# Optimization experiments

Hardware: AMD Instinct MI355X
Metric: run time of the kernel (lower is better)

Reference implementation:

```python
import jax, jax.numpy as jnp
import numpy as np

C_IN = 256


def setup_inputs() -> dict:
    key = jax.random.key(0)
    ks = jax.random.split(key, 10)
    B, C, H, W = 1, C_IN, 96, 96
    Cq = C // 8
    s = 0.05
    return {
        "x": jax.random.normal(ks[0], (B, C, H, W), dtype=jnp.float32),
        "Wq": jax.random.normal(ks[1], (Cq, C), dtype=jnp.float32) * s,
        "bq": jax.random.normal(ks[2], (Cq,), dtype=jnp.float32) * s,
        "Wk": jax.random.normal(ks[3], (Cq, C), dtype=jnp.float32) * s,
        "bk": jax.random.normal(ks[4], (Cq,), dtype=jnp.float32) * s,
        "Wv": jax.random.normal(ks[5], (C, C), dtype=jnp.float32) * s,
        "bv": jax.random.normal(ks[6], (C,), dtype=jnp.float32) * s,
        "W6": jax.random.normal(ks[7], (C, C), dtype=jnp.float32) * s,
        "b6": jax.random.normal(ks[8], (C,), dtype=jnp.float32) * s,
        "gamma": jnp.ones((1,), dtype=jnp.float32),
    }


def reference(x, Wq, bq, Wk, bk, Wv, bv, W6, b6, gamma):
    # TRM forward (OFS just wraps it). 1x1 convs expressed as einsums.
    B, C, H, W = x.shape
    N = H * W
    scale = C ** -0.5  # 1 / sqrt(in_dim)
    xf = x.reshape(B, C, N)
    q = jnp.einsum('oc,bcn->bon', Wq, xf) + bq[None, :, None]   # (B, C/8, N)
    k = jnp.einsum('oc,bcn->bon', Wk, xf) + bk[None, :, None]   # (B, C/8, N)
    v = jnp.einsum('oc,bcn->bon', Wv, xf) + bv[None, :, None]   # (B, C,   N)
    # energy[b,n,m] = sum_c q[b,c,n] * k[b,c,m]  -> full spatial attention (B,N,N)
    energy = jnp.einsum('bcn,bcm->bnm', q, k)
    att = jax.nn.softmax(energy, axis=-1)
    # out[b,c,n] = sum_m v[b,c,m] * att[b,n,m]
    out = jnp.einsum('bcm,bnm->bcn', v, att)                    # (B, C, N)
    # torch: out.permute(2,0,1) -> (N,B,C); max/mean over C; sum; mean over B
    out_co = out.max(axis=1) + out.mean(axis=1)                 # (B, N)
    x_co = out_co.mean(axis=0).reshape(B, -1) * scale           # valid because B == 1
    x_co = jax.nn.softmax(x_co, axis=-1).reshape(B, 1, H, W)    # spatial gate
    gated = x * x_co
    y = jnp.einsum('oc,bchw->bohw', W6, gated) + b6[None, :, None, None]
    return gamma * y + x + y
```

## Files before the change

kernel.cpp:

```cpp
#include <hip/hip_runtime.h>

#define N 9216
#define CIN 256
#define DQ 32
#define NT 144
#define LOG2E 1.44269504088896340736f

typedef short short8 __attribute__((ext_vector_type(8)));
typedef float floatx4 __attribute__((ext_vector_type(4)));
typedef unsigned short ushort_t;

__device__ __forceinline__ ushort_t f2bf(float f) {
  union { float f; unsigned u; } a; a.f = f;
  unsigned u = a.u;
  u += 0x7fffu + ((u >> 16) & 1u);
  return (ushort_t)(u >> 16);
}
__device__ __forceinline__ ushort_t f2bf_fast(float f) {
  union { float f; unsigned u; } a; a.f = f;
  return (ushort_t)((a.u + 0x8000u) >> 16);
}
__device__ __forceinline__ float bf2f(ushort_t h) {
  union { unsigned u; float f; } a; a.u = ((unsigned)h) << 16;
  return a.f;
}

#define ACC4(R, W, XV)                                                   \
  acc[R][0] += (W) * (XV).x;  acc[R][1] += (W) * (XV).y;                 \
  acc[R][2] += (W) * (XV).z;  acc[R][3] += (W) * (XV).w;

__global__ __launch_bounds__(256) void qkv_kernel(
    const float* __restrict__ x,
    const float* __restrict__ Wq, const float* __restrict__ bq,
    const float* __restrict__ Wk, const float* __restrict__ bk,
    const float* __restrict__ Wv, const float* __restrict__ bv,
    ushort_t* __restrict__ qT, ushort_t* __restrict__ kT,
    ushort_t* __restrict__ vG, float* __restrict__ sumExp)
{
  if (blockIdx.x == 0 && blockIdx.y == 0 && threadIdx.x == 0) *sumExp = 0.f;

  __shared__ float xs[64][68];
  const int t = threadIdx.x;
  const int n0 = blockIdx.x * 64;
  const int oc = blockIdx.y;
  const int i = t >> 4, j = t & 15;
  const int o0 = oc * 64 + i * 4;

  const float *W0, *W1, *W2, *W3;
  float b0, b1, b2, b3;
  {
    const int o = o0;
    if (oc == 0) {
      if (o < 32) { W0 = Wq + o*CIN; W1 = Wq + (o+1)*CIN; W2 = Wq + (o+2)*CIN; W3 = Wq + (o+3)*CIN;
                    b0 = bq[o]; b1 = bq[o+1]; b2 = bq[o+2]; b3 = bq[o+3]; }
      else        { W0 = Wk + (o-32)*CIN; W1 = Wk + (o-31)*CIN; W2 = Wk + (o-30)*CIN; W3 = Wk + (o-29)*CIN;
                    b0 = bk[o-32]; b1 = bk[o-31]; b2 = bk[o-30]; b3 = bk[o-29]; }
    } else        { W0 = Wv + (o-64)*CIN; W1 = Wv + (o-63)*CIN; W2 = Wv + (o-62)*CIN; W3 = Wv + (o-61)*CIN;
                    b0 = bv[o-64]; b1 = bv[o-63]; b2 = bv[o-62]; b3 = bv[o-61]; }
  }

  float acc[4][4] = {};
  for (int cc = 0; cc < 4; ++cc) {
    {
      const int row = t >> 2, cq = t & 3;
      const float* src = x + (size_t)(cc * 64 + row) * N + n0 + cq * 16;
      float4 a0 = *(const float4*)(src + 0);
      float4 a1 = *(const float4*)(src + 4);
      float4 a2 = *(const float4*)(src + 8);
      float4 a3 = *(const float4*)(src + 12);
      float* dst = &xs[row][cq * 16];
      *(float4*)(dst + 0) = a0; *(float4*)(dst + 4)  = a1;
      *(float4*)(dst + 8) = a2; *(float4*)(dst + 12) = a3;
    }
    __syncthreads();
#pragma unroll 4
    for (int k4 = 0; k4 < 16; ++k4) {
      const float4 w0 = *(const float4*)(W0 + cc * 64 + k4 * 4);
      const float4 w1 = *(const float4*)(W1 + cc * 64 + k4 * 4);
      const float4 w2 = *(const float4*)(W2 + cc * 64 + k4 * 4);
      const float4 w3 = *(const float4*)(W3 + cc * 64 + k4 * 4);
      const float4 x0 = *(const float4*)&xs[k4 * 4 + 0][j * 4];
      const float4 x1 = *(const float4*)&xs[k4 * 4 + 1][j * 4];
      const float4 x2 = *(const float4*)&xs[k4 * 4 + 2][j * 4];
      const float4 x3 = *(const float4*)&xs[k4 * 4 + 3][j * 4];
      ACC4(0, w0.x, x0) ACC4(0, w0.y, x1) ACC4(0, w0.z, x2) ACC4(0, w0.w, x3)
      ACC4(1, w1.x, x0) ACC4(1, w1.y, x1) ACC4(1, w1.z, x2) ACC4(1, w1.w, x3)
      ACC4(2, w2.x, x0) ACC4(2, w2.y, x1) ACC4(2, w2.z, x2) ACC4(2, w2.w, x3)
      ACC4(3, w3.x, x0) ACC4(3, w3.y, x1) ACC4(3, w3.z, x2) ACC4(3, w3.w, x3)
    }
    __syncthreads();
  }

  const float bias[4] = {b0, b1, b2, b3};
#pragma unroll
  for (int r = 0; r < 4; ++r) {
    const int o = o0 + r;
#pragma unroll
    for (int c = 0; c < 4; ++c) {
      const int n = n0 + j * 4 + c;
      const float val = acc[r][c] + bias[r];
      if (oc == 0) {
        if (o < 32) qT[(size_t)n * DQ + o]        = f2bf(val * LOG2E);
        else        kT[(size_t)n * DQ + (o - 32)] = f2bf(val);
      } else        vG[(size_t)(o - 64) * N + n]  = f2bf(val);
    }
  }
}

__global__ __launch_bounds__(256, 4) void attn_kernel(
    const ushort_t* __restrict__ qT, const ushort_t* __restrict__ kT,
    const ushort_t* __restrict__ vG,
    ushort_t* __restrict__ Opart, float* __restrict__ lpart,
    int base, int rem)
{
  __shared__ ushort_t Pb[2][64][36];

  const int t = threadIdx.x;
  const int w = t >> 6;
  const int lane = t & 63;
  const int quad = lane >> 4;
  const int l15 = lane & 15;
  const int nt = blockIdx.x;
  const int s  = blockIdx.y;
  const int n0 = nt * 64;
  const int sliceIters = base + (s < rem ? 1 : 0);
  const int it0 = s * base + (s < rem ? s : rem);
  const int mbase = it0 * 32;
  const int cw = w * 64;

  short8 aq = *(const short8*)(qT + (size_t)(n0 + 16 * w + l15) * DQ + 8 * quad);

  floatx4 acc[4][4];
#pragma unroll
  for (int a2 = 0; a2 < 4; ++a2)
#pragma unroll
    for (int b2 = 0; b2 < 4; ++b2)
      acc[a2][b2] = (floatx4){0.f, 0.f, 0.f, 0.f};
  float lsum[4] = {0.f, 0.f, 0.f, 0.f};
  const floatx4 z4 = {0.f, 0.f, 0.f, 0.f};

  for (int it = 0; it < sliceIters; ++it) {
    const int m0 = mbase + it * 32;

    short8 kb0 = *(const short8*)(kT + (size_t)(m0 + l15) * DQ + 8 * quad);
    short8 kb1 = *(const short8*)(kT + (size_t)(m0 + 16 + l15) * DQ + 8 * quad);
    floatx4 s0 = __builtin_amdgcn_mfma_f32_16x16x32_bf16(aq, kb0, z4, 0, 0, 0);
    floatx4 s1 = __builtin_amdgcn_mfma_f32_16x16x32_bf16(aq, kb1, z4, 0, 0, 0);

    const ushort_t* vb = vG + (size_t)m0 + 8 * quad;
    short8 av0 = *(const short8*)(vb + (size_t)(cw +  0 + l15) * N);
    short8 av1 = *(const short8*)(vb + (size_t)(cw + 16 + l15) * N);
    short8 av2 = *(const short8*)(vb + (size_t)(cw + 32 + l15) * N);
    short8 av3 = *(const short8*)(vb + (size_t)(cw + 48 + l15) * N);

    ushort_t* pb = &Pb[it & 1][0][0];
#pragma unroll
    for (int r = 0; r < 4; ++r) {
      float p0 = exp2f(s0[r]);
      float p1 = exp2f(s1[r]);
      lsum[r] += p0 + p1;
      const int row = 16 * w + 4 * quad + r;
      pb[row * 36 + l15]      = f2bf_fast(p0);
      pb[row * 36 + 16 + l15] = f2bf_fast(p1);
    }
    __syncthreads();

#pragma unroll
    for (int b2 = 0; b2 < 4; ++b2) {
      const ushort_t* pr = pb + (b2 * 16 + l15) * 36 + 8 * quad;
      union { uint2 u2[2]; short8 v; } u;
      u.u2[0] = *(const uint2*)(pr);
      u.u2[1] = *(const uint2*)(pr + 4);
      const short8 pf = u.v;
      acc[0][b2] = __builtin_amdgcn_mfma_f32_16x16x32_bf16(av0, pf, acc[0][b2], 0, 0, 0);
      acc[1][b2] = __builtin_amdgcn_mfma_f32_16x16x32_bf16(av1, pf, acc[1][b2], 0, 0, 0);
      acc[2][b2] = __builtin_amdgcn_mfma_f32_16x16x32_bf16(av2, pf, acc[2][b2], 0, 0, 0);
      acc[3][b2] = __builtin_amdgcn_mfma_f32_16x16x32_bf16(av3, pf, acc[3][b2], 0, 0, 0);
    }
  }

#pragma unroll
  for (int r = 0; r < 4; ++r) {
    float v = lsum[r];
    v += __shfl_xor(v, 1);
    v += __shfl_xor(v, 2);
    v += __shfl_xor(v, 4);
    v += __shfl_xor(v, 8);
    lsum[r] = v;
  }
  if (l15 == 0) {
#pragma unroll
    for (int r = 0; r < 4; ++r)
      lpart[(size_t)s * N + n0 + 16 * w + 4 * quad + r] = lsum[r];
  }

  const size_t basep = ((size_t)s * NT + nt) * 256;
#pragma unroll
  for (int a2 = 0; a2 < 4; ++a2)
#pragma unroll
    for (int b2 = 0; b2 < 4; ++b2)
#pragma unroll
      for (int r = 0; r < 4; ++r) {
        const int c  = cw + a2 * 16 + 4 * quad + r;
        const int nl = b2 * 16 + l15;
        Opart[(basep + c) * 64 + nl] = f2bf(acc[a2][b2][r]);
      }
}

template<int NSL>
__global__ __launch_bounds__(1024) void cco_kernel(
    const ushort_t* __restrict__ Opart, const float* __restrict__ lpart,
    float* __restrict__ e_buf, float* __restrict__ sumExp)
{
  const int nt = blockIdx.x;
  const int t = threadIdx.x;
  const int n = t & 63, ci = t >> 6;
  float mx = -3.4e38f, sm = 0.f;
#pragma unroll
  for (int k = 0; k < 16; ++k) {
    const int c = ci * 16 + k;
    float val = 0.f;
#pragma unroll
    for (int s2 = 0; s2 < NSL; ++s2)
      val += bf2f(Opart[(((size_t)s2 * NT + nt) * 256 + c) * 64 + n]);
    mx = fmaxf(mx, val);
    sm += val;
  }
  __shared__ float rmx[16][64], rsm[16][64];
  rmx[ci][n] = mx; rsm[ci][n] = sm;
  __syncthreads();
  if (t < 64) {
    float m = rmx[0][t], s = rsm[0][t];
#pragma unroll
    for (int g = 1; g < 16; ++g) { m = fmaxf(m, rmx[g][t]); s += rsm[g][t]; }
    float l = 0.f;
#pragma unroll
    for (int s3 = 0; s3 < NSL; ++s3) l += lpart[(size_t)s3 * N + nt * 64 + t];
    const float oc = (m + s * (1.0f / 256.0f)) / l;
    const float ev = exp2f(oc * (0.0625f * LOG2E));
    e_buf[nt * 64 + t] = ev;
    float vs = ev;
    vs += __shfl_xor(vs, 1);  vs += __shfl_xor(vs, 2);
    vs += __shfl_xor(vs, 4);  vs += __shfl_xor(vs, 8);
    vs += __shfl_xor(vs, 16); vs += __shfl_xor(vs, 32);
    if (t == 0) atomicAdd(sumExp, vs);
  }
}

__global__ __launch_bounds__(256) void final_kernel(
    const float* __restrict__ x, const float* __restrict__ W6,
    const float* __restrict__ b6, const float* __restrict__ gamma,
    const float* __restrict__ e_buf, const float* __restrict__ sumExp,
    float* __restrict__ out)
{
  __shared__ float xs[64][68];
  const int t = threadIdx.x;
  const int n0 = blockIdx.x * 64;
  const int i = t >> 4, j = t & 15;
  const int o0 = blockIdx.y * 64 + i * 4;

  const float* W0 = W6 + (size_t)(o0 + 0) * CIN;
  const float* W1 = W6 + (size_t)(o0 + 1) * CIN;
  const float* W2 = W6 + (size_t)(o0 + 2) * CIN;
  const float* W3 = W6 + (size_t)(o0 + 3) * CIN;

  float acc[4][4] = {};
  for (int cc = 0; cc < 4; ++cc) {
    {
      const int row = t >> 2, cq = t & 3;
      const float* src = x + (size_t)(cc * 64 + row) * N + n0 + cq * 16;
      float4 a0 = *(const float4*)(src + 0);
      float4 a1 = *(const float4*)(src + 4);
      float4 a2 = *(const float4*)(src + 8);
      float4 a3 = *(const float4*)(src + 12);
      float* dst = &xs[row][cq * 16];
      *(float4*)(dst + 0) = a0; *(float4*)(dst + 4)  = a1;
      *(float4*)(dst + 8) = a2; *(float4*)(dst + 12) = a3;
    }
    __syncthreads();
#pragma unroll 4
    for (int k4 = 0; k4 < 16; ++k4) {
      const float4 w0 = *(const float4*)(W0 + cc * 64 + k4 * 4);
      const float4 w1 = *(const float4*)(W1 + cc * 64 + k4 * 4);
      const float4 w2 = *(const float4*)(W2 + cc * 64 + k4 * 4);
      const float4 w3 = *(const float4*)(W3 + cc * 64 + k4 * 4);
      const float4 x0 = *(const float4*)&xs[k4 * 4 + 0][j * 4];
      const float4 x1 = *(const float4*)&xs[k4 * 4 + 1][j * 4];
      const float4 x2 = *(const float4*)&xs[k4 * 4 + 2][j * 4];
      const float4 x3 = *(const float4*)&xs[k4 * 4 + 3][j * 4];
      ACC4(0, w0.x, x0) ACC4(0, w0.y, x1) ACC4(0, w0.z, x2) ACC4(0, w0.w, x3)
      ACC4(1, w1.x, x0) ACC4(1, w1.y, x1) ACC4(1, w1.z, x2) ACC4(1, w1.w, x3)
      ACC4(2, w2.x, x0) ACC4(2, w2.y, x1) ACC4(2, w2.z, x2) ACC4(2, w2.w, x3)
      ACC4(3, w3.x, x0) ACC4(3, w3.y, x1) ACC4(3, w3.z, x2) ACC4(3, w3.w, x3)
    }
    __syncthreads();
  }

  const float g1 = 1.0f + gamma[0];
  const float inv = 1.0f / sumExp[0];
  float4 xc = *(const float4*)(e_buf + n0 + j * 4);
  xc.x *= inv; xc.y *= inv; xc.z *= inv; xc.w *= inv;
#pragma unroll
  for (int r = 0; r < 4; ++r) {
    const int o = o0 + r;
    const float bv6 = b6[o];
    const float4 xrow = *(const float4*)(x + (size_t)o * N + n0 + j * 4);
    float4 res;
    res.x = xrow.x + g1 * (xc.x * acc[r][0] + bv6);
    res.y = xrow.y + g1 * (xc.y * acc[r][1] + bv6);
    res.z = xrow.z + g1 * (xc.z * acc[r][2] + bv6);
    res.w = xrow.w + g1 * (xc.w * acc[r][3] + bv6);
    *(float4*)(out + (size_t)o * N + n0 + j * 4) = res;
  }
}

extern "C" void kernel_launch(void* const* d_in, const int* in_sizes, int n_in,
                              void* d_out, int out_size, void* d_ws, size_t ws_size,
                              hipStream_t stream)
{
  const float* x     = (const float*)d_in[0];
  const float* Wq    = (const float*)d_in[1];
  const float* bq    = (const float*)d_in[2];
  const float* Wk    = (const float*)d_in[3];
  const float* bk    = (const float*)d_in[4];
  const float* Wv    = (const float*)d_in[5];
  const float* bv    = (const float*)d_in[6];
  const float* W6    = (const float*)d_in[7];
  const float* b6    = (const float*)d_in[8];
  const float* gamma = (const float*)d_in[9];
  float* out = (float*)d_out;

  const size_t fixed = (size_t)N * DQ * 2 * 2
                     + (size_t)CIN * N * 2
                     + (size_t)N * 4
                     + 256;
  int nsl = 7;
  size_t need = fixed + (size_t)nsl * NT * 256 * 64 * 2 + (size_t)nsl * N * 4;
  if (ws_size < need) nsl = 4;
  const int totIters = N / 32;
  const int base = totIters / nsl;
  const int rem  = totIters % nsl;

  char* ws = (char*)d_ws;
  const size_t OFF_QT = 0;
  const size_t OFF_KT = OFF_QT + (size_t)N * DQ * 2;
  const size_t OFF_V  = OFF_KT + (size_t)N * DQ * 2;
  const size_t OFF_OP = OFF_V  + (size_t)CIN * N * 2;
  const size_t OFF_LP = OFF_OP + (size_t)nsl * NT * 256 * 64 * 2;
  const size_t OFF_EB = OFF_LP + (size_t)nsl * N * 4;
  const size_t OFF_SE = OFF_EB + (size_t)N * 4;

  ushort_t* qT     = (ushort_t*)(ws + OFF_QT);
  ushort_t* kT     = (ushort_t*)(ws + OFF_KT);
  ushort_t* vG     = (ushort_t*)(ws + OFF_V);
  ushort_t* Opart  = (ushort_t*)(ws + OFF_OP);
  float*    lpart  = (float*)(ws + OFF_LP);
  float*    e_buf  = (float*)(ws + OFF_EB);
  float*    sumExp = (float*)(ws + OFF_SE);

  qkv_kernel<<<dim3(NT, 5), 256, 0, stream>>>(x, Wq, bq, Wk, bk, Wv, bv, qT, kT, vG, sumExp);
  attn_kernel<<<dim3(NT, nsl), 256, 0, stream>>>(qT, kT, vG, Opart, lpart, base, rem);
  if (nsl == 7) cco_kernel<7><<<NT, 1024, 0, stream>>>(Opart, lpart, e_buf, sumExp);
  else          cco_kernel<4><<<NT, 1024, 0, stream>>>(Opart, lpart, e_buf, sumExp);
  final_kernel<<<dim3(NT, 4), 256, 0, stream>>>(x, W6, b6, gamma, e_buf, sumExp, out);
}
```

Measured before the change: 244.0 us.

## Use bf16 MFMA for QKV projection and final 1x1 conv kernels

Replaces the scalar-FMA fp32 GEMMs in the QKV projection and the final W6 projection with bf16 MFMA 16x16x32 instructions. The x tile is converted to bf16 once and staged transposed in shared memory, and the weights are converted to bf16 on the fly from global memory. Each block now stages the full 256-channel tile at once instead of looping over four chunks with syncs. This cuts ALU work in the two projection kernels, which are small next to the attention kernel. It lowers precision of both projections to bf16, and the final kernel's stores become scalar and strided per lane.

Measured after the change: 220.5 us. 1.11x faster.

```diff
diff --git a/kernel.cpp b/kernel.cpp
--- a/kernel.cpp
+++ b/kernel.cpp
@@ -24,12 +24,49 @@
   union { unsigned u; float f; } a; a.u = ((unsigned)h) << 16;
   return a.f;
 }
-
-#define ACC4(R, W, XV)                                                   \
-  acc[R][0] += (W) * (XV).x;  acc[R][1] += (W) * (XV).y;                 \
-  acc[R][2] += (W) * (XV).z;  acc[R][3] += (W) * (XV).w;
-
-__global__ __launch_bounds__(256) void qkv_kernel(
+__device__ __forceinline__ unsigned pack2(float lo, float hi) {
+  return ((unsigned)f2bf_fast(hi) << 16) | (unsigned)f2bf_fast(lo);
+}
+__device__ __forceinline__ short8 mk_bf16x8(const float* p) {
+  float4 f0 = *(const float4*)(p);
+  float4 f1 = *(const float4*)(p + 4);
+  union { unsigned u[4]; short8 v; } r;
+  r.u[0] = pack2(f0.x, f0.y);
+  r.u[1] = pack2(f0.z, f0.w);
+  r.u[2] = pack2(f1.x, f1.y);
+  r.u[3] = pack2(f1.z, f1.w);
+  return r.v;
+}
+
+#define XBT_STRIDE 264
+
+__device__ __forceinline__ void stage_x_tile(
+    const float* __restrict__ x, int n0, int t, ushort_t (*xbT)[XBT_STRIDE])
+{
+  const int p = t & 31, ng = t >> 5;
+  unsigned* base = (unsigned*)&xbT[0][0] + (size_t)(ng * 8) * 132;
+#pragma unroll
+  for (int cc = 0; cc < 4; ++cc) {
+    const int c = cc * 64 + 2 * p;
+    const float* r0 = x + (size_t)c * N + n0 + ng * 8;
+    const float* r1 = r0 + N;
+    float4 a0 = *(const float4*)(r0);
+    float4 a1 = *(const float4*)(r0 + 4);
+    float4 b0 = *(const float4*)(r1);
+    float4 b1 = *(const float4*)(r1 + 4);
+    unsigned* d = base + (cc * 32 + p);
+    d[0 * 132] = pack2(a0.x, b0.x);
+    d[1 * 132] = pack2(a0.y, b0.y);
+    d[2 * 132] = pack2(a0.z, b0.z);
+    d[3 * 132] = pack2(a0.w, b0.w);
+    d[4 * 132] = pack2(a1.x, b1.x);
+    d[5 * 132] = pack2(a1.y, b1.y);
+    d[6 * 132] = pack2(a1.z, b1.z);
+    d[7 * 132] = pack2(a1.w, b1.w);
+  }
+}
+
+__global__ __launch_bounds__(256) void qkv_mfma(
     const float* __restrict__ x,
     const float* __restrict__ Wq, const float* __restrict__ bq,
     const float* __restrict__ Wk, const float* __restrict__ bk,
@@ -39,70 +76,48 @@
 {
   if (blockIdx.x == 0 && blockIdx.y == 0 && threadIdx.x == 0) *sumExp = 0.f;
 
-  __shared__ float xs[64][68];
+  __shared__ ushort_t xbT[64][XBT_STRIDE];
   const int t = threadIdx.x;
   const int n0 = blockIdx.x * 64;
   const int oc = blockIdx.y;
-  const int i = t >> 4, j = t & 15;
-  const int o0 = oc * 64 + i * 4;
-
-  const float *W0, *W1, *W2, *W3;
-  float b0, b1, b2, b3;
-  {
-    const int o = o0;
-    if (oc == 0) {
-      if (o < 32) { W0 = Wq + o*CIN; W1 = Wq + (o+1)*CIN; W2 = Wq + (o+2)*CIN; W3 = Wq + (o+3)*CIN;
-                    b0 = bq[o]; b1 = bq[o+1]; b2 = bq[o+2]; b3 = bq[o+3]; }
-      else        { W0 = Wk + (o-32)*CIN; W1 = Wk + (o-31)*CIN; W2 = Wk + (o-30)*CIN; W3 = Wk + (o-29)*CIN;
-                    b0 = bk[o-32]; b1 = bk[o-31]; b2 = bk[o-30]; b3 = bk[o-29]; }
-    } else        { W0 = Wv + (o-64)*CIN; W1 = Wv + (o-63)*CIN; W2 = Wv + (o-62)*CIN; W3 = Wv + (o-61)*CIN;
-                    b0 = bv[o-64]; b1 = bv[o-63]; b2 = bv[o-62]; b3 = bv[o-61]; }
-  }
-
-  float acc[4][4] = {};
-  for (int cc = 0; cc < 4; ++cc) {
-    {
-      const int row = t >> 2, cq = t & 3;
-      const float* src = x + (size_t)(cc * 64 + row) * N + n0 + cq * 16;
-      float4 a0 = *(const float4*)(src + 0);
-      float4 a1 = *(const float4*)(src + 4);
-      float4 a2 = *(const float4*)(src + 8);
-      float4 a3 = *(const float4*)(src + 12);
-      float* dst = &xs[row][cq * 16];
-      *(float4*)(dst + 0) = a0; *(float4*)(dst + 4)  = a1;
-      *(float4*)(dst + 8) = a2; *(float4*)(dst + 12) = a3;
-    }
-    __syncthreads();
-#pragma unroll 4
-    for (int k4 = 0; k4 < 16; ++k4) {
-      const float4 w0 = *(const float4*)(W0 + cc * 64 + k4 * 4);
-      const float4 w1 = *(const float4*)(W1 + cc * 64 + k4 * 4);
-      const float4 w2 = *(const float4*)(W2 + cc * 64 + k4 * 4);
-      const float4 w3 = *(const float4*)(W3 + cc * 64 + k4 * 4);
-      const float4 x0 = *(const float4*)&xs[k4 * 4 + 0][j * 4];
-      const float4 x1 = *(const float4*)&xs[k4 * 4 + 1][j * 4];
-      const float4 x2 = *(const float4*)&xs[k4 * 4 + 2][j * 4];
-      const float4 x3 = *(const float4*)&xs[k4 * 4 + 3][j * 4];
-      ACC4(0, w0.x, x0) ACC4(0, w0.y, x1) ACC4(0, w0.z, x2) ACC4(0, w0.w, x3)
-      ACC4(1, w1.x, x0) ACC4(1, w1.y, x1) ACC4(1, w1.z, x2) ACC4(1, w1.w, x3)
-      ACC4(2, w2.x, x0) ACC4(2, w2.y, x1) ACC4(2, w2.z, x2) ACC4(2, w2.w, x3)
-      ACC4(3, w3.x, x0) ACC4(3, w3.y, x1) ACC4(3, w3.z, x2) ACC4(3, w3.w, x3)
-    }
-    __syncthreads();
-  }
-
-  const float bias[4] = {b0, b1, b2, b3};
-#pragma unroll
-  for (int r = 0; r < 4; ++r) {
-    const int o = o0 + r;
-#pragma unroll
-    for (int c = 0; c < 4; ++c) {
-      const int n = n0 + j * 4 + c;
-      const float val = acc[r][c] + bias[r];
+  const int w = t >> 6, lane = t & 63;
+  const int quad = lane >> 4, l15 = lane & 15;
+
+  stage_x_tile(x, n0, t, xbT);
+  __syncthreads();
+
+  const int obase = oc * 64 + w * 16;
+  const int oA = obase + l15;
+  const float* Arow;
+  if (oc == 0) Arow = (obase < 32) ? (Wq + (size_t)oA * CIN)
+                                   : (Wk + (size_t)(oA - 32) * CIN);
+  else         Arow = Wv + (size_t)(oA - 64) * CIN;
+
+  floatx4 acc[4];
+#pragma unroll
+  for (int b2 = 0; b2 < 4; ++b2) acc[b2] = (floatx4){0.f, 0.f, 0.f, 0.f};
+
+#pragma unroll
+  for (int ks = 0; ks < 8; ++ks) {
+    const short8 af = mk_bf16x8(Arow + ks * 32 + 8 * quad);
+#pragma unroll
+    for (int b2 = 0; b2 < 4; ++b2) {
+      const short8 bf = *(const short8*)&xbT[b2 * 16 + l15][ks * 32 + 8 * quad];
+      acc[b2] = __builtin_amdgcn_mfma_f32_16x16x32_bf16(af, bf, acc[b2], 0, 0, 0);
+    }
+  }
+
+#pragma unroll
+  for (int b2 = 0; b2 < 4; ++b2) {
+    const int n = n0 + b2 * 16 + l15;
+#pragma unroll
+    for (int r = 0; r < 4; ++r) {
+      const int o = obase + 4 * quad + r;
+      const float val = acc[b2][r];
       if (oc == 0) {
-        if (o < 32) qT[(size_t)n * DQ + o]        = f2bf(val * LOG2E);
-        else        kT[(size_t)n * DQ + (o - 32)] = f2bf(val);
-      } else        vG[(size_t)(o - 64) * N + n]  = f2bf(val);
+        if (o < 32) qT[(size_t)n * DQ + o]        = f2bf((val + bq[o]) * LOG2E);
+        else        kT[(size_t)n * DQ + (o - 32)] = f2bf(val + bk[o - 32]);
+      } else        vG[(size_t)(o - 64) * N + n]  = f2bf(val + bv[o - 64]);
     }
   }
 }
@@ -247,70 +262,50 @@
   }
 }
 
-__global__ __launch_bounds__(256) void final_kernel(
+__global__ __launch_bounds__(256) void final_mfma(
     const float* __restrict__ x, const float* __restrict__ W6,
     const float* __restrict__ b6, const float* __restrict__ gamma,
     const float* __restrict__ e_buf, const float* __restrict__ sumExp,
     float* __restrict__ out)
 {
-  __shared__ float xs[64][68];
+  __shared__ ushort_t xbT[64][XBT_STRIDE];
   const int t = threadIdx.x;
   const int n0 = blockIdx.x * 64;
-  const int i = t >> 4, j = t & 15;
-  const int o0 = blockIdx.y * 64 + i * 4;
-
-  const float* W0 = W6 + (size_t)(o0 + 0) * CIN;
-  const float* W1 = W6 + (size_t)(o0 + 1) * CIN;
-  const float* W2 = W6 + (size_t)(o0 + 2) * CIN;
-  const float* W3 = W6 + (size_t)(o0 + 3) * CIN;
-
-  float acc[4][4] = {};
-  for (int cc = 0; cc < 4; ++cc) {
-    {
-      const int row = t >> 2, cq = t & 3;
-      const float* src = x + (size_t)(cc * 64 + row) * N + n0 + cq * 16;
-      float4 a0 = *(const float4*)(src + 0);
-      float4 a1 = *(const float4*)(src + 4);
-      float4 a2 = *(const float4*)(src + 8);
-      float4 a3 = *(const float4*)(src + 12);
-      float* dst = &xs[row][cq * 16];
-      *(float4*)(dst + 0) = a0; *(float4*)(dst + 4)  = a1;
-      *(float4*)(dst + 8) = a2; *(float4*)(dst + 12) = a3;
-    }
-    __syncthreads();
-#pragma unroll 4
-    for (int k4 = 0; k4 < 16; ++k4) {
-      const float4 w0 = *(const float4*)(W0 + cc * 64 + k4 * 4);
-      const float4 w1 = *(const float4*)(W1 + cc * 64 + k4 * 4);
-      const float4 w2 = *(const float4*)(W2 + cc * 64 + k4 * 4);
-      const float4 w3 = *(const float4*)(W3 + cc * 64 + k4 * 4);
-      const float4 x0 = *(const float4*)&xs[k4 * 4 + 0][j * 4];
-      const float4 x1 = *(const float4*)&xs[k4 * 4 + 1][j * 4];
-      const float4 x2 = *(const float4*)&xs[k4 * 4 + 2][j * 4];
-      const float4 x3 = *(const float4*)&xs[k4 * 4 + 3][j * 4];
-      ACC4(0, w0.x, x0) ACC4(0, w0.y, x1) ACC4(0, w0.z, x2) ACC4(0, w0.w, x3)
-      ACC4(1, w1.x, x0) ACC4(1, w1.y, x1) ACC4(1, w1.z, x2) ACC4(1, w1.w, x3)
-      ACC4(2, w2.x, x0) ACC4(2, w2.y, x1) ACC4(2, w2.z, x2) ACC4(2, w2.w, x3)
-      ACC4(3, w3.x, x0) ACC4(3, w3.y, x1) ACC4(3, w3.z, x2) ACC4(3, w3.w, x3)
-    }
-    __syncthreads();
+  const int w = t >> 6, lane = t & 63;
+  const int quad = lane >> 4, l15 = lane & 15;
+
+  stage_x_tile(x, n0, t, xbT);
+  __syncthreads();
+
+  const int obase = blockIdx.y * 64 + w * 16;
+  const float* Arow = W6 + (size_t)(obase + l15) * CIN;
+
+  floatx4 acc[4];
+#pragma unroll
+  for (int b2 = 0; b2 < 4; ++b2) acc[b2] = (floatx4){0.f, 0.f, 0.f, 0.f};
+
+#pragma unroll
+  for (int ks = 0; ks < 8; ++ks) {
+    const short8 af = mk_bf16x8(Arow + ks * 32 + 8 * quad);
+#pragma unroll
+    for (int b2 = 0; b2 < 4; ++b2) {
+      const short8 bf = *(const short8*)&xbT[b2 * 16 + l15][ks * 32 + 8 * quad];
+      acc[b2] = __builtin_amdgcn_mfma_f32_16x16x32_bf16(af, bf, acc[b2], 0, 0, 0);
+    }
   }
 
   const float g1 = 1.0f + gamma[0];
   const float inv = 1.0f / sumExp[0];
-  float4 xc = *(const float4*)(e_buf + n0 + j * 4);
-  xc.x *= inv; xc.y *= inv; xc.z *= inv; xc.w *= inv;
-#pragma unroll
-  for (int r = 0; r < 4; ++r) {
-    const int o = o0 + r;
-    const float bv6 = b6[o];
-    const float4 xrow = *(const float4*)(x + (size_t)o * N + n0 + j * 4);
-    float4 res;
-    res.x = xrow.x + g1 * (xc.x * acc[r][0] + bv6);
-    res.y = xrow.y + g1 * (xc.y * acc[r][1] + bv6);
-    res.z = xrow.z + g1 * (xc.z * acc[r][2] + bv6);
-    res.w = xrow.w + g1 * (xc.w * acc[r][3] + bv6);
-    *(float4*)(out + (size_t)o * N + n0 + j * 4) = res;
+#pragma unroll
+  for (int b2 = 0; b2 < 4; ++b2) {
+    const int n = n0 + b2 * 16 + l15;
+    const float xc = e_buf[n] * inv;
+#pragma unroll
+    for (int r = 0; r < 4; ++r) {
+      const int o = obase + 4 * quad + r;
+      const float xv = x[(size_t)o * N + n];
+      out[(size_t)o * N + n] = xv + g1 * (xc * acc[b2][r] + b6[o]);
+    }
   }
 }
 
@@ -358,9 +353,9 @@
   float*    e_buf  = (float*)(ws + OFF_EB);
   float*    sumExp = (float*)(ws + OFF_SE);
 
-  qkv_kernel<<<dim3(NT, 5), 256, 0, stream>>>(x, Wq, bq, Wk, bk, Wv, bv, qT, kT, vG, sumExp);
+  qkv_mfma<<<dim3(NT, 5), 256, 0, stream>>>(x, Wq, bq, Wk, bk, Wv, bv, qT, kT, vG, sumExp);
   attn_kernel<<<dim3(NT, nsl), 256, 0, stream>>>(qT, kT, vG, Opart, lpart, base, rem);
   if (nsl == 7) cco_kernel<7><<<NT, 1024, 0, stream>>>(Opart, lpart, e_buf, sumExp);
   else          cco_kernel<4><<<NT, 1024, 0, stream>>>(Opart, lpart, e_buf, sumExp);
-  final_kernel<<<dim3(NT, 4), 256, 0, stream>>>(x, W6, b6, gamma, e_buf, sumExp, out);
-}
+  final_mfma<<<dim3(NT, 4), 256, 0, stream>>>(x, W6, b6, gamma, e_buf, sumExp, out);
+}
```
